# Kernel optimization log

Measured on AMD Instinct MI355X. Metric: run time of the kernel, lower is better.

## Reference

```python
import jax, jax.numpy as jnp
import numpy as np

N, E, S, A, IN, H, OUT = 100000, 400000, 20000, 16, 32, 64, 1
NNZ_SS = 160000
CUR_T, CUR_W = 37, 3


def _gelu(x):
    return jax.nn.gelu(x, approximate=False)  # torch F.gelu default = exact erf


def _spmm(row, col, val, M, nseg):
    # sparse [nseg, K] (COO) @ dense M [K, H]
    return jax.ops.segment_sum(val[:, None] * M[col], row, num_segments=nseg)


def _seg_softmax(logits, seg, nseg):
    mx = jax.ops.segment_max(logits, seg, num_segments=nseg)
    mx = jnp.where(jnp.isfinite(mx), mx, 0.0)  # empty segments -> -inf
    ex = jnp.exp(logits - mx[seg])
    den = jax.ops.segment_sum(ex, seg, num_segments=nseg)
    return ex / (den[seg] + 1e-16)  # PyG softmax epsilon


def _gatv2(x, src, dst, eproj, Wl, bl, Wr, br, att, bias, n):
    # PyG GATv2Conv, heads=1, share_weights=False, negative_slope=0.2
    xl = x @ Wl + bl
    xr = x @ Wr + br
    m = xl[src] + xr[dst] + eproj                      # [nnz, H]
    e = jax.nn.leaky_relu(m, 0.2)
    alpha = _seg_softmax(e @ att, dst, n)              # softmax over in-edges per dst
    return jax.ops.segment_sum(alpha[:, None] * xl[src], dst, num_segments=n) + bias


def _forward(fl, edge_index, se_row, se_col, sn_row, sn_col, ss_row, ss_col, cur_t, cur_w):
    (x_rec, attr, se_val, sn_val, ss_val,
     node_embed, edge_embed, segment_embed, time_embed, week_embed,
     node_lin_W, node_lin_b, attr1_W, attr1_b, attr2_W, attr2_b,
     c1_Wl, c1_bl, c1_Wr, c1_br, c1_We, c1_att, c1_bias,
     c2_Wl, c2_bl, c2_Wr, c2_br, c2_We, c2_att, c2_bias,
     c3_Wl, c3_bl, c3_Wr, c3_br, c3_We, c3_att, c3_bias,
     lin1_W, lin1_b, lin2_W, lin2_b, out_W, out_b) = fl
    src, dst = edge_index[0], edge_index[1]
    attr_f = attr @ attr1_W + attr1_b                  # shared edge feature [E, H]
    # conv1 stack over node_embed with GELU + residual-to-initial
    h = node_embed
    pre = h
    for l in range(3):
        ep = attr_f @ c1_We[l]
        h = _gelu(_gatv2(h, src, dst, ep, c1_Wl[l], c1_bl[l], c1_Wr[l], c1_br[l], c1_att[l], c1_bias[l], N)) + pre
    # conv2 stack over projected recent features
    nf = _gelu(x_rec @ node_lin_W + node_lin_b)
    pre = nf
    for l in range(3):
        ep = attr_f @ c2_We[l]
        nf = _gelu(_gatv2(nf, src, dst, ep, c2_Wl[l], c2_bl[l], c2_Wr[l], c2_br[l], c2_att[l], c2_bias[l], N)) + pre
    # sparse segment aggregations
    x1e = _spmm(se_row, se_col, se_val, edge_embed, S)
    x2e = _spmm(se_row, se_col, se_val, attr @ attr2_W + attr2_b, S)
    x1n = _spmm(sn_row, sn_col, sn_val, h, S)
    x2n = _spmm(sn_row, sn_col, sn_val, nf, S)
    t = jnp.tile(time_embed[cur_t][None, :], (S, 1))
    w = jnp.tile(week_embed[cur_w][None, :], (S, 1))
    xf = jnp.concatenate([segment_embed, x1e, x2e, x1n, x2n, t, w], axis=1)  # [S, 7H]
    # conv3 over segment graph, edge_dim=1 (sparse values as edge attr)
    ep3 = ss_val[:, None] @ c3_We                                            # [nnz_ss, H]
    xf_gnn = _gelu(_gatv2(xf, ss_row, ss_col, ep3, c3_Wl, c3_bl, c3_Wr, c3_br, c3_att, c3_bias, S))
    # MLP head uses only lins[:-1] (as in the source)
    y = _gelu(xf @ lin1_W + lin1_b)
    y = _gelu(y @ lin2_W + lin2_b)
    out = jax.nn.sigmoid(jnp.concatenate([y, xf_gnn], axis=1) @ out_W + out_b) * 3600.0
    return out


def setup_inputs():
    key = jax.random.key(0)
    ks = jax.random.split(key, 64)
    it = iter(range(64))
    def nk():
        return ks[next(it)]
    def p(shape, s=0.05):
        return jax.random.normal(nk(), shape, jnp.float32) * s
    d = {}
    d["x_rec"] = jax.random.normal(nk(), (N, IN), jnp.float32)
    d["attr"] = jax.random.normal(nk(), (E, A), jnp.float32)
    d["se_val"] = jax.random.uniform(nk(), (E,), jnp.float32)
    d["sn_val"] = jax.random.uniform(nk(), (E,), jnp.float32)
    d["ss_val"] = jax.random.uniform(nk(), (NNZ_SS,), jnp.float32)
    d["node_embed"] = p((N, H))
    d["edge_embed"] = p((E, H))
    d["segment_embed"] = p((S, H))
    d["time_embed"] = p((96, H))
    d["week_embed"] = p((7, H))
    d["node_lin_W"] = p((IN, H)); d["node_lin_b"] = p((H,))
    d["attr1_W"] = p((A, H)); d["attr1_b"] = p((H,))
    d["attr2_W"] = p((A, H)); d["attr2_b"] = p((H,))
    for c in ("c1", "c2"):
        d[c + "_Wl"] = p((3, H, H)); d[c + "_bl"] = p((3, H))
        d[c + "_Wr"] = p((3, H, H)); d[c + "_br"] = p((3, H))
        d[c + "_We"] = p((3, H, H))
        d[c + "_att"] = p((3, H)); d[c + "_bias"] = p((3, H))
    d["c3_Wl"] = p((7 * H, H)); d["c3_bl"] = p((H,))
    d["c3_Wr"] = p((7 * H, H)); d["c3_br"] = p((H,))
    d["c3_We"] = p((1, H))
    d["c3_att"] = p((H,)); d["c3_bias"] = p((H,))
    d["lin1_W"] = p((7 * H, H)); d["lin1_b"] = p((H,))
    d["lin2_W"] = p((H, H)); d["lin2_b"] = p((H,))
    d["out_W"] = p((2 * H, OUT)); d["out_b"] = p((OUT,))
    d["edge_index"] = jax.random.randint(nk(), (2, E), 0, N)
    d["se_row"] = jax.random.randint(nk(), (E,), 0, S)
    d["se_col"] = jax.random.randint(nk(), (E,), 0, E)
    d["sn_row"] = jax.random.randint(nk(), (E,), 0, S)
    d["sn_col"] = jax.random.randint(nk(), (E,), 0, N)
    d["ss_row"] = jax.random.randint(nk(), (NNZ_SS,), 0, S)
    d["ss_col"] = jax.random.randint(nk(), (NNZ_SS,), 0, S)
    d["cur_t"] = CUR_T
    d["cur_w"] = CUR_W
    return d


def reference(x_rec, attr, se_val, sn_val, ss_val, node_embed, edge_embed, segment_embed, time_embed, week_embed, node_lin_W, node_lin_b, attr1_W, attr1_b, attr2_W, attr2_b, c1_Wl, c1_bl, c1_Wr, c1_br, c1_We, c1_att, c1_bias, c2_Wl, c2_bl, c2_Wr, c2_br, c2_We, c2_att, c2_bias, c3_Wl, c3_bl, c3_Wr, c3_br, c3_We, c3_att, c3_bias, lin1_W, lin1_b, lin2_W, lin2_b, out_W, out_b, edge_index, se_row, se_col, sn_row, sn_col, ss_row, ss_col, cur_t, cur_w):
    fl = (x_rec, attr, se_val, sn_val, ss_val, node_embed, edge_embed, segment_embed, time_embed, week_embed, node_lin_W, node_lin_b, attr1_W, attr1_b, attr2_W, attr2_b, c1_Wl, c1_bl, c1_Wr, c1_br, c1_We, c1_att, c1_bias, c2_Wl, c2_bl, c2_Wr, c2_br, c2_We, c2_att, c2_bias, c3_Wl, c3_bl, c3_Wr, c3_br, c3_We, c3_att, c3_bias, lin1_W, lin1_b, lin2_W, lin2_b, out_W, out_b)
    return _forward(fl, edge_index, se_row, se_col, sn_row, sn_col, ss_row, ss_col, cur_t, cur_w)
```

## Files before the change

kernel.cpp:

```cpp
#include <hip/hip_runtime.h>
#include <hip/hip_bf16.h>
#include <math.h>

#define DEV __device__ __forceinline__
typedef unsigned short u16;
typedef unsigned int u32;
typedef __attribute__((ext_vector_type(8))) short bf16x8;
typedef __attribute__((ext_vector_type(4))) float f32x4;

DEV float gelu_f(float x) { return 0.5f * x * (1.f + erff(x * 0.70710678118654752f)); }
DEV int rfl(int v) { return __builtin_amdgcn_readfirstlane(v); }
DEV float rflf(float v) {
  int i = __builtin_amdgcn_readfirstlane(__float_as_int(v));
  return __int_as_float(i);
}
DEV u16 f2b(float x) { __hip_bfloat16 h = __float2bfloat16(x); return *reinterpret_cast<u16*>(&h); }
DEV float b2f(u16 u) { __hip_bfloat16 h; *reinterpret_cast<u16*>(&h) = u; return __bfloat162float(h); }
DEV u32 pack2(float a, float b) { return (u32)f2b(a) | ((u32)f2b(b) << 16); }
DEV float blo(u32 u) { return __int_as_float((int)(u << 16)); }
DEV float bhi(u32 u) { return __int_as_float((int)(u & 0xffff0000u)); }

__global__ void fill_zero(float* __restrict__ p, long n) {
  long i = (long)blockIdx.x * blockDim.x + threadIdx.x;
  long st = (long)gridDim.x * blockDim.x;
  for (; i < n; i += st) p[i] = 0.f;
}

__global__ void cvt_all(const float* __restrict__ ne, const float* __restrict__ ee,
                        u16* __restrict__ NE, u16* __restrict__ EE,
                        long nNE, long nEE) {
  long total = nNE + nEE;
  long i = (long)blockIdx.x * blockDim.x + threadIdx.x;
  long st = (long)gridDim.x * blockDim.x;
  for (; i < total; i += st) {
    if (i < nNE) NE[i] = f2b(ne[i]);
    else         EE[i - nNE] = f2b(ee[i - nNE]);
  }
}

__global__ void hist4_k(const int* __restrict__ k1, const int* __restrict__ k2,
                        const int* __restrict__ k3, const int* __restrict__ k4,
                        int E, int Z,
                        int* __restrict__ c1, int* __restrict__ c2,
                        int* __restrict__ c3, int* __restrict__ c4) {
  long total = 3L * E + Z;
  long i = (long)blockIdx.x * blockDim.x + threadIdx.x;
  long st = (long)gridDim.x * blockDim.x;
  for (; i < total; i += st) {
    if (i < E)               atomicAdd(&c1[k1[i]], 1);
    else if (i < 2L * E)     atomicAdd(&c2[k2[i - E]], 1);
    else if (i < 3L * E)     atomicAdd(&c3[k3[i - 2L * E]], 1);
    else                     atomicAdd(&c4[k4[i - 3L * E]], 1);
  }
}

__global__ __launch_bounds__(256) void scan_p1f(
    const int* __restrict__ c1, const int* __restrict__ c2,
    const int* __restrict__ c3, const int* __restrict__ c4,
    int n1, int nS, int nb1, int nbS,
    int* __restrict__ b1, int* __restrict__ b2,
    int* __restrict__ b3, int* __restrict__ b4) {
  int blk = blockIdx.x;
  const int* cnt; int* bsum; int n; int lb;
  if (blk < nb1)                { cnt = c1; bsum = b1; n = n1; lb = blk; }
  else if (blk < nb1 + nbS)     { cnt = c2; bsum = b2; n = nS; lb = blk - nb1; }
  else if (blk < nb1 + 2 * nbS) { cnt = c3; bsum = b3; n = nS; lb = blk - nb1 - nbS; }
  else                          { cnt = c4; bsum = b4; n = nS; lb = blk - nb1 - 2 * nbS; }
  __shared__ int ts[256];
  int base = lb * 1024;
  int s = 0;
  #pragma unroll
  for (int k = 0; k < 4; ++k) {
    int g = base + threadIdx.x * 4 + k;
    if (g < n) s += cnt[g];
  }
  ts[threadIdx.x] = s;
  __syncthreads();
  for (int d = 128; d; d >>= 1) {
    if (threadIdx.x < d) ts[threadIdx.x] += ts[threadIdx.x + d];
    __syncthreads();
  }
  if (threadIdx.x == 0) bsum[lb] = ts[0];
}

__global__ __launch_bounds__(256) void scan_p2f(
    int* __restrict__ b1, int* __restrict__ b2, int* __restrict__ b3, int* __restrict__ b4,
    int nb1, int nbS,
    int* __restrict__ rp1, int* __restrict__ rp2, int* __restrict__ rp3, int* __restrict__ rp4,
    int n1, int nS) {
  int g = blockIdx.x;
  int* bsum = g == 0 ? b1 : g == 1 ? b2 : g == 2 ? b3 : b4;
  int* rp   = g == 0 ? rp1 : g == 1 ? rp2 : g == 2 ? rp3 : rp4;
  int nb    = g == 0 ? nb1 : nbS;
  int n     = g == 0 ? n1 : nS;
  __shared__ int ts[256];
  int tid = threadIdx.x;
  int v = (tid < nb) ? bsum[tid] : 0;
  ts[tid] = v;
  __syncthreads();
  for (int d = 1; d < 256; d <<= 1) {
    int w = (tid >= d) ? ts[tid - d] : 0;
    __syncthreads();
    ts[tid] += w;
    __syncthreads();
  }
  if (tid < nb) bsum[tid] = (tid == 0) ? 0 : ts[tid - 1];
  if (tid == 255) rp[n] = ts[255];
}

__global__ __launch_bounds__(256) void scan_p3f(
    const int* __restrict__ c1, const int* __restrict__ c2,
    const int* __restrict__ c3, const int* __restrict__ c4,
    int n1, int nS, int nb1, int nbS,
    const int* __restrict__ b1, const int* __restrict__ b2,
    const int* __restrict__ b3, const int* __restrict__ b4,
    int* __restrict__ rp1, int* __restrict__ rp2,
    int* __restrict__ rp3, int* __restrict__ rp4,
    int* __restrict__ q1, int* __restrict__ q2,
    int* __restrict__ q3, int* __restrict__ q4) {
  int blk = blockIdx.x;
  const int* cnt; const int* bsum; int* rp; int* cursor; int n; int lb;
  if (blk < nb1)                { cnt = c1; bsum = b1; rp = rp1; cursor = q1; n = n1; lb = blk; }
  else if (blk < nb1 + nbS)     { cnt = c2; bsum = b2; rp = rp2; cursor = q2; n = nS; lb = blk - nb1; }
  else if (blk < nb1 + 2 * nbS) { cnt = c3; bsum = b3; rp = rp3; cursor = q3; n = nS; lb = blk - nb1 - nbS; }
  else                          { cnt = c4; bsum = b4; rp = rp4; cursor = q4; n = nS; lb = blk - nb1 - 2 * nbS; }
  __shared__ int ts[256];
  int base = lb * 1024;
  int tid = threadIdx.x;
  int c[4];
  int s = 0;
  #pragma unroll
  for (int k = 0; k < 4; ++k) {
    int g = base + tid * 4 + k;
    c[k] = (g < n) ? cnt[g] : 0;
    s += c[k];
  }
  ts[tid] = s;
  __syncthreads();
  for (int d = 1; d < 256; d <<= 1) {
    int w = (tid >= d) ? ts[tid - d] : 0;
    __syncthreads();
    ts[tid] += w;
    __syncthreads();
  }
  int run = bsum[lb] + ((tid == 0) ? 0 : ts[tid - 1]);
  #pragma unroll
  for (int k = 0; k < 4; ++k) {
    int g = base + tid * 4 + k;
    if (g < n) {
      rp[g] = run;
      cursor[g] = run;
      run += c[k];
    }
  }
}

__global__ void scat4_k(
    const int* __restrict__ edst, const int* __restrict__ esrc,
    const float* __restrict__ attr,
    const int* __restrict__ se_row, const int* __restrict__ se_col, const float* __restrict__ se_val,
    const int* __restrict__ sn_row, const int* __restrict__ sn_col, const float* __restrict__ sn_val,
    const int* __restrict__ ss_col, const int* __restrict__ ss_row, const float* __restrict__ ss_val,
    int E, int Z,
    int* __restrict__ q1, int* __restrict__ q2, int* __restrict__ q3, int* __restrict__ q4,
    int* __restrict__ src1s, u16* __restrict__ atrs,
    int* __restrict__ col2s, float* __restrict__ val2s,
    int* __restrict__ col3s, float* __restrict__ val3s,
    int* __restrict__ src4s, float* __restrict__ val4s) {
  long total = 3L * E + Z;
  long i = (long)blockIdx.x * blockDim.x + threadIdx.x;
  long st = (long)gridDim.x * blockDim.x;
  for (; i < total; i += st) {
    if (i < E) {
      int p = atomicAdd(&q1[edst[i]], 1);
      src1s[p] = esrc[i];
      const float* sr = attr + (size_t)i * 16;
      u32* dr = (u32*)(atrs + (size_t)p * 16);
      #pragma unroll
      for (int k = 0; k < 8; ++k) dr[k] = pack2(sr[2 * k], sr[2 * k + 1]);
    } else if (i < 2L * E) {
      long j = i - E;
      int p = atomicAdd(&q2[se_row[j]], 1);
      col2s[p] = se_col[j]; val2s[p] = se_val[j];
    } else if (i < 3L * E) {
      long j = i - 2L * E;
      int p = atomicAdd(&q3[sn_row[j]], 1);
      col3s[p] = sn_col[j]; val3s[p] = sn_val[j];
    } else {
      long j = i - 3L * E;
      int p = atomicAdd(&q4[ss_col[j]], 1);
      src4s[p] = ss_row[j]; val4s[p] = ss_val[j];
    }
  }
}

__global__ __launch_bounds__(256) void compose_we(
    const float* __restrict__ a1W, const float* __restrict__ a1b,
    const float* __restrict__ c1We, const float* __restrict__ c2We,
    float* __restrict__ WEC, float* __restrict__ BEC)
{
  int l = blockIdx.x;
  const float* We = (l < 3) ? (c1We + l * 4096) : (c2We + (l - 3) * 4096);
  __shared__ float wes[4096];
  int tid = threadIdx.x;
  for (int i = tid; i < 4096; i += 256) wes[i] = We[i];
  __syncthreads();
  for (int i = tid; i < 1024; i += 256) {
    int k = i >> 6, j = i & 63;
    float s = 0.f;
    #pragma unroll 16
    for (int m = 0; m < 64; ++m) s += a1W[k * 64 + m] * wes[m * 64 + j];
    WEC[l * 1024 + i] = s;
  }
  if (tid < 64) {
    float s = 0.f;
    for (int m = 0; m < 64; ++m) s += a1b[m] * wes[m * 64 + tid];
    BEC[l * 64 + tid] = s;
  }
}

__global__ __launch_bounds__(256) void prep_wt(
    const float* __restrict__ c1Wl, const float* __restrict__ c1Wr,
    const float* __restrict__ c2Wl, const float* __restrict__ c2Wr,
    const float* __restrict__ nodeW, const float* __restrict__ c3Wl,
    const float* __restrict__ c3Wr, const float* __restrict__ lin1W,
    const float* __restrict__ lin2W, u16* __restrict__ WTS)
{
  long idx = (long)blockIdx.x * 256 + threadIdx.x;
  if (idx >= 141312) return;
  float v;
  if (idx < 49152) {
    const float* src = (idx < 12288) ? c1Wl : (idx < 24576) ? c1Wr : (idx < 36864) ? c2Wl : c2Wr;
    long loc = idx & 12287;
    long m = loc >> 12;
    int c = (int)((loc >> 6) & 63), k = (int)(loc & 63);
    v = src[m * 4096 + k * 64 + c];
  } else if (idx < 51200) {
    long loc = idx - 49152;
    int c = (int)(loc >> 5), k = (int)(loc & 31);
    v = nodeW[k * 64 + c];
  } else if (idx < 137216) {
    long base = (idx < 79872) ? 51200 : (idx < 108544) ? 79872 : 108544;
    const float* src = (idx < 79872) ? c3Wl : (idx < 108544) ? c3Wr : lin1W;
    long loc = idx - base;
    int c = (int)(loc / 448), k = (int)(loc % 448);
    v = src[k * 64 + c];
  } else {
    long loc = idx - 137216;
    int c = (int)(loc >> 6), k = (int)(loc & 63);
    v = lin2W[k * 64 + c];
  }
  WTS[idx] = f2b(v);
}

template <int ACT, bool PAIR, bool XBF, bool OBF, bool DUAL>
__global__ __launch_bounds__(256) void gemm_mfma(
    const void* __restrict__ Xv, int nrows, int K,
    const u16* __restrict__ WT1, const float* __restrict__ b1, void* __restrict__ O1v,
    const u16* __restrict__ WT2, const float* __restrict__ b2, void* __restrict__ O2v,
    const void* __restrict__ Xv2,
    const u16* __restrict__ WT3, const float* __restrict__ b3, void* __restrict__ O3v,
    const u16* __restrict__ WT4, const float* __restrict__ b4, void* __restrict__ O4v)
{
  __shared__ __align__(16) u16 xs[4096];
  __shared__ __align__(16) u16 ws1[4096];
  __shared__ __align__(16) u16 ws2[PAIR ? 4096 : 8];

  int bid = blockIdx.x;
  const void* X_ = Xv;
  const u16* w1p = WT1; const float* b1p = b1; void* o1p = O1v;
  const u16* w2p = WT2; const float* b2p = b2; void* o2p = O2v;
  if constexpr (DUAL) {
    int half = gridDim.x >> 1;
    if (bid >= half) {
      bid -= half;
      X_ = Xv2;
      w1p = WT3; b1p = b3; o1p = O3v;
      w2p = WT4; b2p = b4; o2p = O4v;
    }
  }

  const int tid = threadIdx.x;
  const int row0 = bid * 64;
  const int wid = tid >> 6, lane = tid & 63;
  const int lrow = lane & 15, lgrp = lane >> 4;
  const int r0 = wid * 16;
  const int sr = tid >> 2;
  const int sq = tid & 3;
  const int ssw = sr & 7;

  f32x4 acc[4];
  f32x4 acc2[PAIR ? 4 : 1];
  #pragma unroll
  for (int f = 0; f < 4; ++f) { acc[f] = (f32x4)0.f; if constexpr (PAIR) acc2[f] = (f32x4)0.f; }

  for (int kc = 0; kc < K; kc += 64) {
    __syncthreads();
    {
      int gr = row0 + sr;
      int kb = kc + sq * 16;
      uint4 pa, pb;
      if constexpr (XBF) {
        const u16* X = (const u16*)X_;
        if (gr < nrows && kb + 16 <= K) {
          pa = *(const uint4*)&X[(size_t)gr * K + kb];
          pb = *(const uint4*)&X[(size_t)gr * K + kb + 8];
        } else {
          u32 p[8];
          #pragma unroll
          for (int i = 0; i < 8; ++i) {
            u16 a = (gr < nrows && kb + 2 * i < K)     ? X[(size_t)gr * K + kb + 2 * i]     : (u16)0;
            u16 b = (gr < nrows && kb + 2 * i + 1 < K) ? X[(size_t)gr * K + kb + 2 * i + 1] : (u16)0;
            p[i] = (u32)a | ((u32)b << 16);
          }
          pa = make_uint4(p[0], p[1], p[2], p[3]);
          pb = make_uint4(p[4], p[5], p[6], p[7]);
        }
      } else {
        const float* X = (const float*)X_;
        float f[16];
        if (gr < nrows && kb + 16 <= K) {
          #pragma unroll
          for (int i = 0; i < 4; ++i)
            *(float4*)&f[i * 4] = *(const float4*)&X[(size_t)gr * K + kb + i * 4];
        } else {
          #pragma unroll
          for (int i = 0; i < 16; ++i)
            f[i] = (gr < nrows && kb + i < K) ? X[(size_t)gr * K + kb + i] : 0.f;
        }
        u32 p[8];
        #pragma unroll
        for (int i = 0; i < 8; ++i) p[i] = pack2(f[2 * i], f[2 * i + 1]);
        pa = make_uint4(p[0], p[1], p[2], p[3]);
        pb = make_uint4(p[4], p[5], p[6], p[7]);
      }
      *(uint4*)&xs[sr * 64 + (((sq * 2))     ^ ssw) * 8] = pa;
      *(uint4*)&xs[sr * 64 + (((sq * 2 + 1)) ^ ssw) * 8] = pb;
    }
    {
      int kb = kc + sq * 16;
      uint4 qa, qb;
      if (kb + 16 <= K) {
        qa = *(const uint4*)&w1p[(size_t)sr * K + kb];
        qb = *(const uint4*)&w1p[(size_t)sr * K + kb + 8];
      } else {
        u32 p[8];
        #pragma unroll
        for (int i = 0; i < 8; ++i) {
          u16 a = (kb + 2 * i < K)     ? w1p[(size_t)sr * K + kb + 2 * i]     : (u16)0;
          u16 b = (kb + 2 * i + 1 < K) ? w1p[(size_t)sr * K + kb + 2 * i + 1] : (u16)0;
          p[i] = (u32)a | ((u32)b << 16);
        }
        qa = make_uint4(p[0], p[1], p[2], p[3]);
        qb = make_uint4(p[4], p[5], p[6], p[7]);
      }
      *(uint4*)&ws1[sr * 64 + (((sq * 2))     ^ ssw) * 8] = qa;
      *(uint4*)&ws1[sr * 64 + (((sq * 2 + 1)) ^ ssw) * 8] = qb;
      if constexpr (PAIR) {
        if (kb + 16 <= K) {
          qa = *(const uint4*)&w2p[(size_t)sr * K + kb];
          qb = *(const uint4*)&w2p[(size_t)sr * K + kb + 8];
        } else {
          u32 p[8];
          #pragma unroll
          for (int i = 0; i < 8; ++i) {
            u16 a = (kb + 2 * i < K)     ? w2p[(size_t)sr * K + kb + 2 * i]     : (u16)0;
            u16 b = (kb + 2 * i + 1 < K) ? w2p[(size_t)sr * K + kb + 2 * i + 1] : (u16)0;
            p[i] = (u32)a | ((u32)b << 16);
          }
          qa = make_uint4(p[0], p[1], p[2], p[3]);
          qb = make_uint4(p[4], p[5], p[6], p[7]);
        }
        *(uint4*)&ws2[sr * 64 + (((sq * 2))     ^ ssw) * 8] = qa;
        *(uint4*)&ws2[sr * 64 + (((sq * 2 + 1)) ^ ssw) * 8] = qb;
      }
    }
    __syncthreads();
    #pragma unroll
    for (int kh = 0; kh < 2; ++kh) {
      const int g = (4 * kh + lgrp) ^ (lrow & 7);
      bf16x8 a = *(const bf16x8*)&xs[(r0 + lrow) * 64 + g * 8];
      #pragma unroll
      for (int f = 0; f < 4; ++f) {
        int col = f * 16 + lrow;
        bf16x8 b = *(const bf16x8*)&ws1[col * 64 + g * 8];
        acc[f] = __builtin_amdgcn_mfma_f32_16x16x32_bf16(a, b, acc[f], 0, 0, 0);
        if constexpr (PAIR) {
          bf16x8 b2v = *(const bf16x8*)&ws2[col * 64 + g * 8];
          acc2[f] = __builtin_amdgcn_mfma_f32_16x16x32_bf16(a, b2v, acc2[f], 0, 0, 0);
        }
      }
    }
  }

  #pragma unroll
  for (int f = 0; f < 4; ++f) {
    int col = f * 16 + lrow;
    float bv = b1p[col];
    float bv2 = 0.f;
    if constexpr (PAIR) bv2 = b2p[col];
    #pragma unroll
    for (int r = 0; r < 4; ++r) {
      int grow = row0 + r0 + lgrp * 4 + r;
      if (grow >= nrows) continue;
      float v = acc[f][r] + bv;
      if constexpr (ACT == 1) v = gelu_f(v);
      if constexpr (OBF) ((u16*)o1p)[(size_t)grow * 64 + col] = f2b(v);
      else               ((float*)o1p)[(size_t)grow * 64 + col] = v;
      if constexpr (PAIR) {
        float v2 = acc2[f][r] + bv2;
        if constexpr (ACT == 1) v2 = gelu_f(v2);
        if constexpr (OBF) ((u16*)o2p)[(size_t)grow * 64 + col] = f2b(v2);
        else               ((float*)o2p)[(size_t)grow * 64 + col] = v2;
      }
    }
  }
}

__global__ __launch_bounds__(256) void gat_gather2(
    const int* __restrict__ rowptr,
    const int* __restrict__ srcs, const u16* __restrict__ atrs,
    const float* __restrict__ wec1, const float* __restrict__ bec1,
    const float* __restrict__ att1, const float* __restrict__ bias1,
    const float* __restrict__ wec2, const float* __restrict__ bec2,
    const float* __restrict__ att2, const float* __restrict__ bias2,
    const u16* __restrict__ xl1, const u16* __restrict__ xr1,
    const u16* __restrict__ pre1, u16* __restrict__ out1,
    const u16* __restrict__ xl2, const u16* __restrict__ xr2,
    const u16* __restrict__ pre2, u16* __restrict__ out2, int n)
{
  int tid = threadIdx.x;
  int wid = tid >> 6, lane = tid & 63;
  int d = blockIdx.x * 4 + wid;
  if (d >= n) return;
  float w1[16], w2[16];
  #pragma unroll
  for (int k = 0; k < 16; ++k) {
    w1[k] = wec1[k * 64 + lane];
    w2[k] = wec2[k * 64 + lane];
  }
  float be1 = bec1[lane], be2 = bec2[lane];
  float at1 = att1[lane], at2 = att2[lane];
  float xr1v = b2f(xr1[(size_t)d * 64 + lane]);
  float xr2v = b2f(xr2[(size_t)d * 64 + lane]);
  float n1 = 0.f, d1 = 0.f, n2 = 0.f, d2 = 0.f;
  int j0 = rfl(rowptr[d]), j1 = rfl(rowptr[d + 1]);
  int j = j0;
  for (; j + 2 <= j1; j += 2) {
    int sa = rfl(srcs[j]);
    int sb = rfl(srcs[j + 1]);
    const u32* ara = (const u32*)(atrs + (size_t)j * 16);
    const u32* arb = ara + 8;
    float xl1a = b2f(xl1[(size_t)sa * 64 + lane]);
    float xl2a = b2f(xl2[(size_t)sa * 64 + lane]);
    float xl1b = b2f(xl1[(size_t)sb * 64 + lane]);
    float xl2b = b2f(xl2[(size_t)sb * 64 + lane]);
    float ep1a = be1, ep2a = be2, ep1b = be1, ep2b = be2;
    #pragma unroll
    for (int k = 0; k < 8; ++k) {
      u32 pa_ = ara[k], pb_ = arb[k];
      float a0 = blo(pa_), a1 = bhi(pa_);
      float b0 = blo(pb_), b1 = bhi(pb_);
      ep1a += a0 * w1[2 * k] + a1 * w1[2 * k + 1];
      ep2a += a0 * w2[2 * k] + a1 * w2[2 * k + 1];
      ep1b += b0 * w1[2 * k] + b1 * w1[2 * k + 1];
      ep2b += b0 * w2[2 * k] + b1 * w2[2 * k + 1];
    }
    float m1a = xl1a + xr1v + ep1a, m2a = xl2a + xr2v + ep2a;
    float m1b = xl1b + xr1v + ep1b, m2b = xl2b + xr2v + ep2b;
    float l1a = m1a < 0.f ? 0.2f * m1a : m1a;
    float l2a = m2a < 0.f ? 0.2f * m2a : m2a;
    float l1b = m1b < 0.f ? 0.2f * m1b : m1b;
    float l2b = m2b < 0.f ? 0.2f * m2b : m2b;
    float t1a = at1 * l1a, t2a = at2 * l2a, t1b = at1 * l1b, t2b = at2 * l2b;
    #pragma unroll
    for (int o = 32; o; o >>= 1) {
      t1a += __shfl_xor(t1a, o, 64);
      t2a += __shfl_xor(t2a, o, 64);
      t1b += __shfl_xor(t1b, o, 64);
      t2b += __shfl_xor(t2b, o, 64);
    }
    float x1a = __expf(t1a), x2a = __expf(t2a), x1b = __expf(t1b), x2b = __expf(t2b);
    n1 += x1a * xl1a + x1b * xl1b; d1 += x1a + x1b;
    n2 += x2a * xl2a + x2b * xl2b; d2 += x2a + x2b;
  }
  for (; j < j1; ++j) {
    int s = rfl(srcs[j]);
    const u32* arow = (const u32*)(atrs + (size_t)j * 16);
    float xl1v = b2f(xl1[(size_t)s * 64 + lane]);
    float xl2v = b2f(xl2[(size_t)s * 64 + lane]);
    float ep1 = be1, ep2 = be2;
    #pragma unroll
    for (int k = 0; k < 8; ++k) {
      u32 pk = arow[k];
      float a0 = blo(pk), a1 = bhi(pk);
      ep1 += a0 * w1[2 * k] + a1 * w1[2 * k + 1];
      ep2 += a0 * w2[2 * k] + a1 * w2[2 * k + 1];
    }
    float m1 = xl1v + xr1v + ep1;
    float m2 = xl2v + xr2v + ep2;
    float lr1 = m1 < 0.f ? 0.2f * m1 : m1;
    float lr2 = m2 < 0.f ? 0.2f * m2 : m2;
    float t1 = at1 * lr1, t2 = at2 * lr2;
    #pragma unroll
    for (int o = 32; o; o >>= 1) {
      t1 += __shfl_xor(t1, o, 64);
      t2 += __shfl_xor(t2, o, 64);
    }
    float ex1 = __expf(t1), ex2 = __expf(t2);
    n1 += ex1 * xl1v; d1 += ex1;
    n2 += ex2 * xl2v; d2 += ex2;
  }
  size_t base = (size_t)d * 64 + lane;
  float v1 = n1 / (d1 + 1e-16f) + bias1[lane];
  float v2 = n2 / (d2 + 1e-16f) + bias2[lane];
  out1[base] = f2b(gelu_f(v1) + b2f(pre1[base]));
  out2[base] = f2b(gelu_f(v2) + b2f(pre2[base]));
}

__global__ __launch_bounds__(256) void gat_seg_g(
    const int* __restrict__ rowptr, const int* __restrict__ srcs,
    const float* __restrict__ vals,
    const float* __restrict__ we3, const float* __restrict__ att,
    const float* __restrict__ bias,
    const u16* __restrict__ xl, const u16* __restrict__ xr,
    float* __restrict__ out, int n)
{
  int tid = threadIdx.x;
  int wid = tid >> 6, lane = tid & 63;
  int d = blockIdx.x * 4 + wid;
  if (d >= n) return;
  float we3v = we3[lane], attv = att[lane], bsv = bias[lane];
  float xrv = b2f(xr[(size_t)d * 64 + lane]);
  float accn = 0.f, accd = 0.f;
  int j0 = rfl(rowptr[d]), j1 = rfl(rowptr[d + 1]);
  for (int j = j0; j < j1; ++j) {
    int s = rfl(srcs[j]);
    float vv = rflf(vals[j]);
    float ep = vv * we3v;
    float xlv = b2f(xl[(size_t)s * 64 + lane]);
    float m = xlv + xrv + ep;
    float lr = m < 0.f ? 0.2f * m : m;
    float t = attv * lr;
    #pragma unroll
    for (int o = 32; o; o >>= 1) t += __shfl_xor(t, o, 64);
    float ex = __expf(t);
    accn += ex * xlv;
    accd += ex;
  }
  float v = accn / (accd + 1e-16f) + bsv;
  out[(size_t)d * 64 + lane] = gelu_f(v);
}

__global__ __launch_bounds__(256) void xf_build(
    const int* __restrict__ rp2, const int* __restrict__ col2s, const float* __restrict__ val2s,
    const int* __restrict__ rp3, const int* __restrict__ col3s, const float* __restrict__ val3s,
    const u16* __restrict__ EE, const float* __restrict__ attr,
    const float* __restrict__ W2, const float* __restrict__ b2,
    const float* __restrict__ seg_embed, const float* __restrict__ time_embed,
    const float* __restrict__ week_embed,
    const int* __restrict__ cur_t, const int* __restrict__ cur_w,
    const u16* __restrict__ h, const u16* __restrict__ nf,
    float* __restrict__ xf, int S)
{
  __shared__ float ws[1024];
  __shared__ float bs[64];
  int tid = threadIdx.x;
  for (int i = tid; i < 1024; i += 256) ws[i] = W2[i];
  if (tid < 64) bs[tid] = b2[tid];
  __syncthreads();
  int wid = tid >> 6, lane = tid & 63;
  int gw = blockIdx.x * 4 + wid;
  int s = gw >> 1, role = gw & 1;
  if (s >= S) return;
  float* row = xf + (size_t)s * 448;
  if (role == 0) {
    row[lane]       = seg_embed[(size_t)s * 64 + lane];
    row[320 + lane] = time_embed[cur_t[0] * 64 + lane];
    row[384 + lane] = week_embed[cur_w[0] * 64 + lane];
    float acc1 = 0.f, aat = 0.f, vs = 0.f;
    int j0 = rfl(rp2[s]), j1 = rfl(rp2[s + 1]);
    for (int j = j0; j < j1; ++j) {
      int c = rfl(col2s[j]);
      float v = rflf(val2s[j]);
      acc1 += v * b2f(EE[(size_t)c * 64 + lane]);
      aat  += v * attr[(size_t)c * 16 + (lane & 15)];
      vs   += v;
    }
    float x2 = vs * bs[lane];
    #pragma unroll
    for (int k = 0; k < 16; ++k)
      x2 += __shfl(aat, k, 64) * ws[k * 64 + lane];
    row[64 + lane]  = acc1;
    row[128 + lane] = x2;
  } else {
    float acch = 0.f, accf = 0.f;
    int j0 = rfl(rp3[s]), j1 = rfl(rp3[s + 1]);
    for (int j = j0; j < j1; ++j) {
      int c = rfl(col3s[j]);
      float v = rflf(val3s[j]);
      acch += v * b2f(h[(size_t)c * 64 + lane]);
      accf += v * b2f(nf[(size_t)c * 64 + lane]);
    }
    row[192 + lane] = acch;
    row[256 + lane] = accf;
  }
}

__global__ __launch_bounds__(256) void head_k(
    const float* __restrict__ y2, const float* __restrict__ xfg,
    const float* __restrict__ outW, const float* __restrict__ outb,
    float* __restrict__ out, int S)
{
  int wid = threadIdx.x >> 6, lane = threadIdx.x & 63;
  int s = blockIdx.x * 4 + wid;
  if (s >= S) return;
  float t = y2[(size_t)s * 64 + lane] * outW[lane] + xfg[(size_t)s * 64 + lane] * outW[64 + lane];
  #pragma unroll
  for (int o = 32; o; o >>= 1) t += __shfl_xor(t, o, 64);
  if (lane == 0) {
    float z = t + outb[0];
    out[s] = 3600.f / (1.f + __expf(-z));
  }
}

extern "C" void kernel_launch(void* const* d_in, const int* in_sizes, int n_in,
                              void* d_out, int out_size, void* d_ws, size_t ws_size,
                              hipStream_t stream)
{
  const float* x_rec       = (const float*)d_in[0];
  const float* attr        = (const float*)d_in[1];
  const float* se_val      = (const float*)d_in[2];
  const float* sn_val      = (const float*)d_in[3];
  const float* ss_val      = (const float*)d_in[4];
  const float* node_embed  = (const float*)d_in[5];
  const float* edge_embed  = (const float*)d_in[6];
  const float* seg_embed   = (const float*)d_in[7];
  const float* time_embed  = (const float*)d_in[8];
  const float* week_embed  = (const float*)d_in[9];
  const float* node_lin_W  = (const float*)d_in[10];
  const float* node_lin_b  = (const float*)d_in[11];
  const float* attr2_W     = (const float*)d_in[14];
  const float* attr2_b     = (const float*)d_in[15];
  const float* c1_Wl       = (const float*)d_in[16];
  const float* c1_bl       = (const float*)d_in[17];
  const float* c1_Wr       = (const float*)d_in[18];
  const float* c1_br       = (const float*)d_in[19];
  const float* c1_att      = (const float*)d_in[21];
  const float* c1_bias     = (const float*)d_in[22];
  const float* c2_Wl       = (const float*)d_in[23];
  const float* c2_bl       = (const float*)d_in[24];
  const float* c2_Wr       = (const float*)d_in[25];
  const float* c2_br       = (const float*)d_in[26];
  const float* c2_att      = (const float*)d_in[28];
  const float* c2_bias     = (const float*)d_in[29];
  const float* c3_Wl       = (const float*)d_in[30];
  const float* c3_bl       = (const float*)d_in[31];
  const float* c3_Wr       = (const float*)d_in[32];
  const float* c3_br       = (const float*)d_in[33];
  const float* c3_We       = (const float*)d_in[34];
  const float* c3_att      = (const float*)d_in[35];
  const float* c3_bias     = (const float*)d_in[36];
  const float* lin1_W      = (const float*)d_in[37];
  const float* lin1_b      = (const float*)d_in[38];
  const float* lin2_W      = (const float*)d_in[39];
  const float* lin2_b      = (const float*)d_in[40];
  const float* out_W       = (const float*)d_in[41];
  const float* out_b       = (const float*)d_in[42];
  const int* edge_index    = (const int*)d_in[43];
  const int* se_row        = (const int*)d_in[44];
  const int* se_col        = (const int*)d_in[45];
  const int* sn_row        = (const int*)d_in[46];
  const int* sn_col        = (const int*)d_in[47];
  const int* ss_row        = (const int*)d_in[48];
  const int* ss_col        = (const int*)d_in[49];
  const int* cur_t         = (const int*)d_in[50];
  const int* cur_w         = (const int*)d_in[51];

  const int N = in_sizes[0] / 32;
  const int E = in_sizes[1] / 16;
  const int S = in_sizes[7] / 64;
  const int NNZSS = in_sizes[4];

  float* W = (float*)d_ws;
  size_t o = 0;
  u16* A   = (u16*)(W + o); o += (size_t)N * 32;
  u16* B   = (u16*)(W + o); o += (size_t)N * 32;
  u16* A2  = (u16*)(W + o); o += (size_t)N * 32;
  u16* B2  = (u16*)(W + o); o += (size_t)N * 32;
  u16* Hc  = (u16*)(W + o); o += (size_t)N * 32;
  u16* F0  = (u16*)(W + o); o += (size_t)N * 32;
  u16* Fc  = (u16*)(W + o); o += (size_t)N * 32;
  u16* NE  = (u16*)(W + o); o += (size_t)N * 32;
  u16* EE  = (u16*)(W + o); o += (size_t)E * 32;
  u16* ATRS = (u16*)(W + o); o += (size_t)E * 8;
  float* XF  = W + o; o += (size_t)S * 448;
  float* XFG = W + o; o += (size_t)S * 64;
  float* Y   = W + o; o += (size_t)S * 64;
  float* Y2  = W + o; o += (size_t)S * 64;
  float* WEC = W + o; o += 6 * 1024;
  float* BEC = W + o; o += 6 * 64;
  u16* WTS   = (u16*)(W + o); o += 70656;
  float* val2s = W + o; o += E;
  float* val3s = W + o; o += E;
  float* val4s = W + o; o += NNZSS;
  int* I = (int*)(W + o);
  size_t q = 0;
  int* cur1 = I + q; q += N + 1;
  int* cur2 = I + q; q += S + 1;
  int* cur3 = I + q; q += S + 1;
  int* cur4 = I + q; q += S + 1;
  int* rp1  = I + q; q += N + 1;
  int* rp2  = I + q; q += S + 1;
  int* rp3  = I + q; q += S + 1;
  int* rp4  = I + q; q += S + 1;
  int* src1s = I + q; q += E;
  int* col2s = I + q; q += E;
  int* col3s = I + q; q += E;
  int* src4s = I + q; q += NNZSS;
  int* bs1  = I + q; q += 256;
  int* bs2  = I + q; q += 256;
  int* bs3  = I + q; q += 256;
  int* bs4  = I + q; q += 256;

  u16* WT_c1l  = WTS;
  u16* WT_c1r  = WTS + 12288;
  u16* WT_c2l  = WTS + 24576;
  u16* WT_c2r  = WTS + 36864;
  u16* WT_node = WTS + 49152;
  u16* WT_c3l  = WTS + 51200;
  u16* WT_c3r  = WTS + 79872;
  u16* WT_lin1 = WTS + 108544;
  u16* WT_lin2 = WTS + 137216;

  const int* edst = edge_index + E;

  dim3 blk(256);
  const int gN64 = (N + 63) / 64;
  const int gS64 = (S + 63) / 64;
  const int gS4  = (S + 3) / 4;
  const int gN4  = (N + 3) / 4;
  const int gXF  = (2 * S + 3) / 4;
  const int nbN  = (N + 1 + 1023) / 1024;
  const int nbS  = (S + 1 + 1023) / 1024;

  long ztot = (long)(N + 1) + 3L * (S + 1);
  fill_zero<<<256, blk, 0, stream>>>((float*)cur1, ztot);
  prep_wt<<<(141312 + 255) / 256, blk, 0, stream>>>(c1_Wl, c1_Wr, c2_Wl, c2_Wr,
                                                    node_lin_W, c3_Wl, c3_Wr,
                                                    lin1_W, lin2_W, WTS);
  cvt_all<<<2048, blk, 0, stream>>>(node_embed, edge_embed, NE, EE,
                                    (long)N * 64, (long)E * 64);
  hist4_k<<<1024, blk, 0, stream>>>(edst, se_row, sn_row, ss_col, E, NNZSS,
                                    cur1, cur2, cur3, cur4);
  scan_p1f<<<nbN + 3 * nbS, blk, 0, stream>>>(cur1, cur2, cur3, cur4,
                                              N + 1, S + 1, nbN, nbS,
                                              bs1, bs2, bs3, bs4);
  scan_p2f<<<4, blk, 0, stream>>>(bs1, bs2, bs3, bs4, nbN, nbS,
                                  rp1, rp2, rp3, rp4, N, S);
  scan_p3f<<<nbN + 3 * nbS, blk, 0, stream>>>(cur1, cur2, cur3, cur4,
                                              N, S, nbN, nbS,
                                              bs1, bs2, bs3, bs4,
                                              rp1, rp2, rp3, rp4,
                                              cur1, cur2, cur3, cur4);
  scat4_k<<<1024, blk, 0, stream>>>(edst, edge_index, attr,
                                    se_row, se_col, se_val,
                                    sn_row, sn_col, sn_val,
                                    ss_col, ss_row, ss_val,
                                    E, NNZSS,
                                    cur1, cur2, cur3, cur4,
                                    src1s, ATRS, col2s, val2s, col3s, val3s, src4s, val4s);

  compose_we<<<6, blk, 0, stream>>>((const float*)d_in[12], (const float*)d_in[13],
                                    (const float*)d_in[20], (const float*)d_in[27], WEC, BEC);

  gemm_mfma<1, false, false, true, false><<<gN64, blk, 0, stream>>>(x_rec, N, 32,
      WT_node, node_lin_b, F0, nullptr, nullptr, nullptr,
      nullptr, nullptr, nullptr, nullptr, nullptr, nullptr, nullptr);

  for (int l = 0; l < 3; ++l) {
    gemm_mfma<0, true, true, true, true><<<2 * gN64, blk, 0, stream>>>(
        l == 0 ? NE : Hc, N, 64,
        WT_c1l + l * 4096, c1_bl + l * 64, A, WT_c1r + l * 4096, c1_br + l * 64, B,
        l == 0 ? F0 : Fc,
        WT_c2l + l * 4096, c2_bl + l * 64, A2, WT_c2r + l * 4096, c2_br + l * 64, B2);
    gat_gather2<<<gN4, blk, 0, stream>>>(rp1, src1s, ATRS,
        WEC + l * 1024, BEC + l * 64, c1_att + l * 64, c1_bias + l * 64,
        WEC + (3 + l) * 1024, BEC + (3 + l) * 64, c2_att + l * 64, c2_bias + l * 64,
        A, B, NE, Hc,
        A2, B2, F0, Fc, N);
  }

  xf_build<<<gXF, blk, 0, stream>>>(rp2, col2s, val2s, rp3, col3s, val3s,
                                    EE, attr, attr2_W, attr2_b,
                                    seg_embed, time_embed, week_embed, cur_t, cur_w,
                                    Hc, Fc, XF, S);

  gemm_mfma<0, true, false, true, false><<<gS64, blk, 0, stream>>>(XF, S, 448,
      WT_c3l, c3_bl, A, WT_c3r, c3_br, B,
      nullptr, nullptr, nullptr, nullptr, nullptr, nullptr, nullptr);
  gat_seg_g<<<gS4, blk, 0, stream>>>(rp4, src4s, val4s, c3_We, c3_att, c3_bias,
                                     A, B, XFG, S);

  gemm_mfma<1, false, false, false, false><<<gS64, blk, 0, stream>>>(XF, S, 448,
      WT_lin1, lin1_b, Y, nullptr, nullptr, nullptr,
      nullptr, nullptr, nullptr, nullptr, nullptr, nullptr, nullptr);
  gemm_mfma<1, false, false, false, false><<<gS64, blk, 0, stream>>>(Y, S, 64,
      WT_lin2, lin2_b, Y2, nullptr, nullptr, nullptr,
      nullptr, nullptr, nullptr, nullptr, nullptr, nullptr, nullptr);
  head_k<<<gS4, blk, 0, stream>>>(Y2, XFG, out_W, out_b, (float*)d_out, S);
}
```

Baseline: 736.8 us.

## Fuse prep kernels, drop edge_embed bf16 copy, merge lin1 into c3 GEMM

Merges the zero-fill, weight transpose and node_embed conversion into one grid-stride launch. It also stops converting edge_embed to bf16 and reads the fp32 values directly in xf_build, saving a full E x 64 conversion pass. A third weight slot (TRI) lets the c3 GEMM compute lin1 with GELU from the same staged XF tile, removing a second read of XF. The GAT gather stages the edge weights in LDS and switches exp to exp2 with log2e folded into att. The risks are higher LDS and register use in the fused GEMM, which may lower occupancy, and more bandwidth in xf_build from the fp32 reads.

```diff
diff --git a/kernel.cpp b/kernel.cpp
--- a/kernel.cpp
+++ b/kernel.cpp
@@ -20,21 +20,52 @@
 DEV float blo(u32 u) { return __int_as_float((int)(u << 16)); }
 DEV float bhi(u32 u) { return __int_as_float((int)(u & 0xffff0000u)); }
 
-__global__ void fill_zero(float* __restrict__ p, long n) {
-  long i = (long)blockIdx.x * blockDim.x + threadIdx.x;
-  long st = (long)gridDim.x * blockDim.x;
-  for (; i < n; i += st) p[i] = 0.f;
-}
-
-__global__ void cvt_all(const float* __restrict__ ne, const float* __restrict__ ee,
-                        u16* __restrict__ NE, u16* __restrict__ EE,
-                        long nNE, long nEE) {
-  long total = nNE + nEE;
+#define LOG2E 1.44269504088896340736f
+
+__global__ void prep_misc(
+    int* __restrict__ zbase, long ztot,
+    const float* __restrict__ c1Wl, const float* __restrict__ c1Wr,
+    const float* __restrict__ c2Wl, const float* __restrict__ c2Wr,
+    const float* __restrict__ nodeW, const float* __restrict__ c3Wl,
+    const float* __restrict__ c3Wr, const float* __restrict__ lin1W,
+    const float* __restrict__ lin2W, u16* __restrict__ WTS,
+    const float* __restrict__ node_embed, u16* __restrict__ NE, long nNE)
+{
+  long total = ztot + 141312 + nNE;
   long i = (long)blockIdx.x * blockDim.x + threadIdx.x;
   long st = (long)gridDim.x * blockDim.x;
   for (; i < total; i += st) {
-    if (i < nNE) NE[i] = f2b(ne[i]);
-    else         EE[i - nNE] = f2b(ee[i - nNE]);
+    if (i < ztot) {
+      zbase[i] = 0;
+    } else if (i < ztot + 141312) {
+      long idx = i - ztot;
+      float v;
+      if (idx < 49152) {
+        const float* src = (idx < 12288) ? c1Wl : (idx < 24576) ? c1Wr : (idx < 36864) ? c2Wl : c2Wr;
+        long loc = idx & 12287;
+        long m = loc >> 12;
+        int c = (int)((loc >> 6) & 63), k = (int)(loc & 63);
+        v = src[m * 4096 + k * 64 + c];
+      } else if (idx < 51200) {
+        long loc = idx - 49152;
+        int c = (int)(loc >> 5), k = (int)(loc & 31);
+        v = nodeW[k * 64 + c];
+      } else if (idx < 137216) {
+        long base = (idx < 79872) ? 51200 : (idx < 108544) ? 79872 : 108544;
+        const float* src = (idx < 79872) ? c3Wl : (idx < 108544) ? c3Wr : lin1W;
+        long loc = idx - base;
+        int c = (int)(loc / 448), k = (int)(loc % 448);
+        v = src[k * 64 + c];
+      } else {
+        long loc = idx - 137216;
+        int c = (int)(loc >> 6), k = (int)(loc & 63);
+        v = lin2W[k * 64 + c];
+      }
+      WTS[idx] = f2b(v);
+    } else {
+      long j = i - ztot - 141312;
+      NE[j] = f2b(node_embed[j]);
+    }
   }
 }
 
@@ -219,52 +250,20 @@
   }
 }
 
-__global__ __launch_bounds__(256) void prep_wt(
-    const float* __restrict__ c1Wl, const float* __restrict__ c1Wr,
-    const float* __restrict__ c2Wl, const float* __restrict__ c2Wr,
-    const float* __restrict__ nodeW, const float* __restrict__ c3Wl,
-    const float* __restrict__ c3Wr, const float* __restrict__ lin1W,
-    const float* __restrict__ lin2W, u16* __restrict__ WTS)
-{
-  long idx = (long)blockIdx.x * 256 + threadIdx.x;
-  if (idx >= 141312) return;
-  float v;
-  if (idx < 49152) {
-    const float* src = (idx < 12288) ? c1Wl : (idx < 24576) ? c1Wr : (idx < 36864) ? c2Wl : c2Wr;
-    long loc = idx & 12287;
-    long m = loc >> 12;
-    int c = (int)((loc >> 6) & 63), k = (int)(loc & 63);
-    v = src[m * 4096 + k * 64 + c];
-  } else if (idx < 51200) {
-    long loc = idx - 49152;
-    int c = (int)(loc >> 5), k = (int)(loc & 31);
-    v = nodeW[k * 64 + c];
-  } else if (idx < 137216) {
-    long base = (idx < 79872) ? 51200 : (idx < 108544) ? 79872 : 108544;
-    const float* src = (idx < 79872) ? c3Wl : (idx < 108544) ? c3Wr : lin1W;
-    long loc = idx - base;
-    int c = (int)(loc / 448), k = (int)(loc % 448);
-    v = src[k * 64 + c];
-  } else {
-    long loc = idx - 137216;
-    int c = (int)(loc >> 6), k = (int)(loc & 63);
-    v = lin2W[k * 64 + c];
-  }
-  WTS[idx] = f2b(v);
-}
-
-template <int ACT, bool PAIR, bool XBF, bool OBF, bool DUAL>
+template <int ACT, bool PAIR, bool XBF, bool OBF, bool DUAL, bool TRI>
 __global__ __launch_bounds__(256) void gemm_mfma(
     const void* __restrict__ Xv, int nrows, int K,
     const u16* __restrict__ WT1, const float* __restrict__ b1, void* __restrict__ O1v,
     const u16* __restrict__ WT2, const float* __restrict__ b2, void* __restrict__ O2v,
     const void* __restrict__ Xv2,
     const u16* __restrict__ WT3, const float* __restrict__ b3, void* __restrict__ O3v,
-    const u16* __restrict__ WT4, const float* __restrict__ b4, void* __restrict__ O4v)
+    const u16* __restrict__ WT4, const float* __restrict__ b4, void* __restrict__ O4v,
+    const u16* __restrict__ WT5, const float* __restrict__ b5, float* __restrict__ O5v)
 {
   __shared__ __align__(16) u16 xs[4096];
   __shared__ __align__(16) u16 ws1[4096];
   __shared__ __align__(16) u16 ws2[PAIR ? 4096 : 8];
+  __shared__ __align__(16) u16 ws3[TRI ? 4096 : 8];
 
   int bid = blockIdx.x;
   const void* X_ = Xv;
@@ -291,8 +290,13 @@
 
   f32x4 acc[4];
   f32x4 acc2[PAIR ? 4 : 1];
+  f32x4 acc3[TRI ? 4 : 1];
   #pragma unroll
-  for (int f = 0; f < 4; ++f) { acc[f] = (f32x4)0.f; if constexpr (PAIR) acc2[f] = (f32x4)0.f; }
+  for (int f = 0; f < 4; ++f) {
+    acc[f] = (f32x4)0.f;
+    if constexpr (PAIR) acc2[f] = (f32x4)0.f;
+    if constexpr (TRI)  acc3[f] = (f32x4)0.f;
+  }
 
   for (int kc = 0; kc < K; kc += 64) {
     __syncthreads();
@@ -340,40 +344,27 @@
     {
       int kb = kc + sq * 16;
       uint4 qa, qb;
-      if (kb + 16 <= K) {
-        qa = *(const uint4*)&w1p[(size_t)sr * K + kb];
-        qb = *(const uint4*)&w1p[(size_t)sr * K + kb + 8];
-      } else {
-        u32 p[8];
-        #pragma unroll
-        for (int i = 0; i < 8; ++i) {
-          u16 a = (kb + 2 * i < K)     ? w1p[(size_t)sr * K + kb + 2 * i]     : (u16)0;
-          u16 b = (kb + 2 * i + 1 < K) ? w1p[(size_t)sr * K + kb + 2 * i + 1] : (u16)0;
-          p[i] = (u32)a | ((u32)b << 16);
-        }
-        qa = make_uint4(p[0], p[1], p[2], p[3]);
-        qb = make_uint4(p[4], p[5], p[6], p[7]);
-      }
-      *(uint4*)&ws1[sr * 64 + (((sq * 2))     ^ ssw) * 8] = qa;
-      *(uint4*)&ws1[sr * 64 + (((sq * 2 + 1)) ^ ssw) * 8] = qb;
-      if constexpr (PAIR) {
-        if (kb + 16 <= K) {
-          qa = *(const uint4*)&w2p[(size_t)sr * K + kb];
-          qb = *(const uint4*)&w2p[(size_t)sr * K + kb + 8];
-        } else {
-          u32 p[8];
-          #pragma unroll
-          for (int i = 0; i < 8; ++i) {
-            u16 a = (kb + 2 * i < K)     ? w2p[(size_t)sr * K + kb + 2 * i]     : (u16)0;
-            u16 b = (kb + 2 * i + 1 < K) ? w2p[(size_t)sr * K + kb + 2 * i + 1] : (u16)0;
-            p[i] = (u32)a | ((u32)b << 16);
-          }
-          qa = make_uint4(p[0], p[1], p[2], p[3]);
-          qb = make_uint4(p[4], p[5], p[6], p[7]);
-        }
-        *(uint4*)&ws2[sr * 64 + (((sq * 2))     ^ ssw) * 8] = qa;
-        *(uint4*)&ws2[sr * 64 + (((sq * 2 + 1)) ^ ssw) * 8] = qb;
-      }
+      #define STAGE_W(WP, WS)                                                       \
+        if (kb + 16 <= K) {                                                         \
+          qa = *(const uint4*)&WP[(size_t)sr * K + kb];                             \
+          qb = *(const uint4*)&WP[(size_t)sr * K + kb + 8];                         \
+        } else {                                                                    \
+          u32 p[8];                                                                 \
+          _Pragma("unroll")                                                         \
+          for (int i = 0; i < 8; ++i) {                                             \
+            u16 a = (kb + 2 * i < K)     ? WP[(size_t)sr * K + kb + 2 * i]     : (u16)0; \
+            u16 b = (kb + 2 * i + 1 < K) ? WP[(size_t)sr * K + kb + 2 * i + 1] : (u16)0; \
+            p[i] = (u32)a | ((u32)b << 16);                                         \
+          }                                                                         \
+          qa = make_uint4(p[0], p[1], p[2], p[3]);                                  \
+          qb = make_uint4(p[4], p[5], p[6], p[7]);                                  \
+        }                                                                           \
+        *(uint4*)&WS[sr * 64 + (((sq * 2))     ^ ssw) * 8] = qa;                    \
+        *(uint4*)&WS[sr * 64 + (((sq * 2 + 1)) ^ ssw) * 8] = qb;
+      STAGE_W(w1p, ws1)
+      if constexpr (PAIR) { STAGE_W(w2p, ws2) }
+      if constexpr (TRI)  { STAGE_W(WT5, ws3) }
+      #undef STAGE_W
     }
     __syncthreads();
     #pragma unroll
@@ -389,6 +380,10 @@
           bf16x8 b2v = *(const bf16x8*)&ws2[col * 64 + g * 8];
           acc2[f] = __builtin_amdgcn_mfma_f32_16x16x32_bf16(a, b2v, acc2[f], 0, 0, 0);
         }
+        if constexpr (TRI) {
+          bf16x8 b3v = *(const bf16x8*)&ws3[col * 64 + g * 8];
+          acc3[f] = __builtin_amdgcn_mfma_f32_16x16x32_bf16(a, b3v, acc3[f], 0, 0, 0);
+        }
       }
     }
   }
@@ -397,8 +392,9 @@
   for (int f = 0; f < 4; ++f) {
     int col = f * 16 + lrow;
     float bv = b1p[col];
-    float bv2 = 0.f;
+    float bv2 = 0.f, bv3 = 0.f;
     if constexpr (PAIR) bv2 = b2p[col];
+    if constexpr (TRI)  bv3 = b5[col];
     #pragma unroll
     for (int r = 0; r < 4; ++r) {
       int grow = row0 + r0 + lgrp * 4 + r;
@@ -413,6 +409,10 @@
         if constexpr (OBF) ((u16*)o2p)[(size_t)grow * 64 + col] = f2b(v2);
         else               ((float*)o2p)[(size_t)grow * 64 + col] = v2;
       }
+      if constexpr (TRI) {
+        float v3 = gelu_f(acc3[f][r] + bv3);
+        O5v[(size_t)grow * 64 + col] = v3;
+      }
     }
   }
 }
@@ -429,18 +429,24 @@
     const u16* __restrict__ xl2, const u16* __restrict__ xr2,
     const u16* __restrict__ pre2, u16* __restrict__ out2, int n)
 {
+  __shared__ float wlds[2048];
   int tid = threadIdx.x;
+  for (int i = tid; i < 1024; i += 256) {
+    wlds[i] = wec1[i];
+    wlds[1024 + i] = wec2[i];
+  }
+  __syncthreads();
   int wid = tid >> 6, lane = tid & 63;
   int d = blockIdx.x * 4 + wid;
   if (d >= n) return;
   float w1[16], w2[16];
   #pragma unroll
   for (int k = 0; k < 16; ++k) {
-    w1[k] = wec1[k * 64 + lane];
-    w2[k] = wec2[k * 64 + lane];
+    w1[k] = wlds[k * 64 + lane];
+    w2[k] = wlds[1024 + k * 64 + lane];
   }
   float be1 = bec1[lane], be2 = bec2[lane];
-  float at1 = att1[lane], at2 = att2[lane];
+  float at1 = att1[lane] * LOG2E, at2 = att2[lane] * LOG2E;
   float xr1v = b2f(xr1[(size_t)d * 64 + lane]);
   float xr2v = b2f(xr2[(size_t)d * 64 + lane]);
   float n1 = 0.f, d1 = 0.f, n2 = 0.f, d2 = 0.f;
@@ -480,7 +486,7 @@
       t1b += __shfl_xor(t1b, o, 64);
       t2b += __shfl_xor(t2b, o, 64);
     }
-    float x1a = __expf(t1a), x2a = __expf(t2a), x1b = __expf(t1b), x2b = __expf(t2b);
+    float x1a = exp2f(t1a), x2a = exp2f(t2a), x1b = exp2f(t1b), x2b = exp2f(t2b);
     n1 += x1a * xl1a + x1b * xl1b; d1 += x1a + x1b;
     n2 += x2a * xl2a + x2b * xl2b; d2 += x2a + x2b;
   }
@@ -507,7 +513,7 @@
       t1 += __shfl_xor(t1, o, 64);
       t2 += __shfl_xor(t2, o, 64);
     }
-    float ex1 = __expf(t1), ex2 = __expf(t2);
+    float ex1 = exp2f(t1), ex2 = exp2f(t2);
     n1 += ex1 * xl1v; d1 += ex1;
     n2 += ex2 * xl2v; d2 += ex2;
   }
@@ -530,7 +536,7 @@
   int wid = tid >> 6, lane = tid & 63;
   int d = blockIdx.x * 4 + wid;
   if (d >= n) return;
-  float we3v = we3[lane], attv = att[lane], bsv = bias[lane];
+  float we3v = we3[lane], attv = att[lane] * LOG2E, bsv = bias[lane];
   float xrv = b2f(xr[(size_t)d * 64 + lane]);
   float accn = 0.f, accd = 0.f;
   int j0 = rfl(rowptr[d]), j1 = rfl(rowptr[d + 1]);
@@ -544,7 +550,7 @@
     float t = attv * lr;
     #pragma unroll
     for (int o = 32; o; o >>= 1) t += __shfl_xor(t, o, 64);
-    float ex = __expf(t);
+    float ex = exp2f(t);
     accn += ex * xlv;
     accd += ex;
   }
@@ -555,7 +561,7 @@
 __global__ __launch_bounds__(256) void xf_build(
     const int* __restrict__ rp2, const int* __restrict__ col2s, const float* __restrict__ val2s,
     const int* __restrict__ rp3, const int* __restrict__ col3s, const float* __restrict__ val3s,
-    const u16* __restrict__ EE, const float* __restrict__ attr,
+    const float* __restrict__ edge_embed, const float* __restrict__ attr,
     const float* __restrict__ W2, const float* __restrict__ b2,
     const float* __restrict__ seg_embed, const float* __restrict__ time_embed,
     const float* __restrict__ week_embed,
@@ -583,7 +589,7 @@
     for (int j = j0; j < j1; ++j) {
       int c = rfl(col2s[j]);
       float v = rflf(val2s[j]);
-      acc1 += v * b2f(EE[(size_t)c * 64 + lane]);
+      acc1 += v * edge_embed[(size_t)c * 64 + lane];
       aat  += v * attr[(size_t)c * 16 + (lane & 15)];
       vs   += v;
     }
@@ -692,7 +698,6 @@
   u16* F0  = (u16*)(W + o); o += (size_t)N * 32;
   u16* Fc  = (u16*)(W + o); o += (size_t)N * 32;
   u16* NE  = (u16*)(W + o); o += (size_t)N * 32;
-  u16* EE  = (u16*)(W + o); o += (size_t)E * 32;
   u16* ATRS = (u16*)(W + o); o += (size_t)E * 8;
   float* XF  = W + o; o += (size_t)S * 448;
   float* XFG = W + o; o += (size_t)S * 64;
@@ -745,12 +750,10 @@
   const int nbS  = (S + 1 + 1023) / 1024;
 
   long ztot = (long)(N + 1) + 3L * (S + 1);
-  fill_zero<<<256, blk, 0, stream>>>((float*)cur1, ztot);
-  prep_wt<<<(141312 + 255) / 256, blk, 0, stream>>>(c1_Wl, c1_Wr, c2_Wl, c2_Wr,
-                                                    node_lin_W, c3_Wl, c3_Wr,
-                                                    lin1_W, lin2_W, WTS);
-  cvt_all<<<2048, blk, 0, stream>>>(node_embed, edge_embed, NE, EE,
-                                    (long)N * 64, (long)E * 64);
+  prep_misc<<<2048, blk, 0, stream>>>(cur1, ztot,
+                                      c1_Wl, c1_Wr, c2_Wl, c2_Wr,
+                                      node_lin_W, c3_Wl, c3_Wr, lin1_W, lin2_W, WTS,
+                                      node_embed, NE, (long)N * 64);
   hist4_k<<<1024, blk, 0, stream>>>(edst, se_row, sn_row, ss_col, E, NNZSS,
                                     cur1, cur2, cur3, cur4);
   scan_p1f<<<nbN + 3 * nbS, blk, 0, stream>>>(cur1, cur2, cur3, cur4,
@@ -774,16 +777,18 @@
   compose_we<<<6, blk, 0, stream>>>((const float*)d_in[12], (const float*)d_in[13],
                                     (const float*)d_in[20], (const float*)d_in[27], WEC, BEC);
 
-  gemm_mfma<1, false, false, true, false><<<gN64, blk, 0, stream>>>(x_rec, N, 32,
+  gemm_mfma<1, false, false, true, false, false><<<gN64, blk, 0, stream>>>(x_rec, N, 32,
       WT_node, node_lin_b, F0, nullptr, nullptr, nullptr,
-      nullptr, nullptr, nullptr, nullptr, nullptr, nullptr, nullptr);
+      nullptr, nullptr, nullptr, nullptr, nullptr, nullptr, nullptr,
+      nullptr, nullptr, nullptr);
 
   for (int l = 0; l < 3; ++l) {
-    gemm_mfma<0, true, true, true, true><<<2 * gN64, blk, 0, stream>>>(
+    gemm_mfma<0, true, true, true, true, false><<<2 * gN64, blk, 0, stream>>>(
         l == 0 ? NE : Hc, N, 64,
         WT_c1l + l * 4096, c1_bl + l * 64, A, WT_c1r + l * 4096, c1_br + l * 64, B,
         l == 0 ? F0 : Fc,
-        WT_c2l + l * 4096, c2_bl + l * 64, A2, WT_c2r + l * 4096, c2_br + l * 64, B2);
+        WT_c2l + l * 4096, c2_bl + l * 64, A2, WT_c2r + l * 4096, c2_br + l * 64, B2,
+        nullptr, nullptr, nullptr);
     gat_gather2<<<gN4, blk, 0, stream>>>(rp1, src1s, ATRS,
         WEC + l * 1024, BEC + l * 64, c1_att + l * 64, c1_bias + l * 64,
         WEC + (3 + l) * 1024, BEC + (3 + l) * 64, c2_att + l * 64, c2_bias + l * 64,
@@ -792,21 +797,20 @@
   }
 
   xf_build<<<gXF, blk, 0, stream>>>(rp2, col2s, val2s, rp3, col3s, val3s,
-                                    EE, attr, attr2_W, attr2_b,
+                                    edge_embed, attr, attr2_W, attr2_b,
                                     seg_embed, time_embed, week_embed, cur_t, cur_w,
                                     Hc, Fc, XF, S);
 
-  gemm_mfma<0, true, false, true, false><<<gS64, blk, 0, stream>>>(XF, S, 448,
+  gemm_mfma<0, true, false, true, false, true><<<gS64, blk, 0, stream>>>(XF, S, 448,
       WT_c3l, c3_bl, A, WT_c3r, c3_br, B,
-      nullptr, nullptr, nullptr, nullptr, nullptr, nullptr, nullptr);
+      nullptr, nullptr, nullptr, nullptr, nullptr, nullptr, nullptr,
+      WT_lin1, lin1_b, Y);
   gat_seg_g<<<gS4, blk, 0, stream>>>(rp4, src4s, val4s, c3_We, c3_att, c3_bias,
                                      A, B, XFG, S);
 
-  gemm_mfma<1, false, false, false, false><<<gS64, blk, 0, stream>>>(XF, S, 448,
-      WT_lin1, lin1_b, Y, nullptr, nullptr, nullptr,
-      nullptr, nullptr, nullptr, nullptr, nullptr, nullptr, nullptr);
-  gemm_mfma<1, false, false, false, false><<<gS64, blk, 0, stream>>>(Y, S, 64,
+  gemm_mfma<1, false, false, false, false, false><<<gS64, blk, 0, stream>>>(Y, S, 64,
       WT_lin2, lin2_b, Y2, nullptr, nullptr, nullptr,
-      nullptr, nullptr, nullptr, nullptr, nullptr, nullptr, nullptr);
+      nullptr, nullptr, nullptr, nullptr, nullptr, nullptr, nullptr,
+      nullptr, nullptr, nullptr);
   head_k<<<gS4, blk, 0, stream>>>(Y2, XFG, out_W, out_b, (float*)d_out, S);
 }
```

Measured after the change: 848.7 us. 15.2% more time.
